# Performance work log

Hardware: AMD Instinct MI355X
Metric: run time of the kernel (lower is better)

Reference implementation:

```python
import jax, jax.numpy as jnp
import numpy as np

N = 20000          # nodes
E = 320000         # edges (avg degree 16)
D_IN, D1, D2, D_OUT = 256, 512, 256, 64
EPS = 1e-5


def _glorot(key, shape):
    lim = (6.0 / (shape[0] + shape[1])) ** 0.5
    return jax.random.uniform(key, shape, jnp.float32, -lim, lim)


def setup_inputs() -> dict:
    key = jax.random.key(0)
    ks = jax.random.split(key, 8)
    x = jax.random.normal(ks[0], (N, D_IN), jnp.float32)
    edge_index = jax.random.randint(ks[1], (2, E), 0, N, dtype=jnp.int64)
    return {
        "x": x,
        "edge_index": edge_index,
        # SAGEConv 1 (SoftmaxAggregation temperature t1 over inp_dim channels)
        "t1": jnp.ones((1, D_IN), jnp.float32),
        "Wl1": _glorot(ks[2], (D_IN, D1)), "bl1": jnp.zeros((D1,), jnp.float32),
        "Wr1": _glorot(ks[3], (D_IN, D1)),
        "g1": jnp.ones((D1,), jnp.float32), "beta1": jnp.zeros((D1,), jnp.float32),
        # SAGEConv 2
        "t2": jnp.ones((1, D1), jnp.float32),
        "Wl2": _glorot(ks[4], (D1, D2)), "bl2": jnp.zeros((D2,), jnp.float32),
        "Wr2": _glorot(ks[5], (D1, D2)),
        "g2": jnp.ones((D2,), jnp.float32), "beta2": jnp.zeros((D2,), jnp.float32),
        # final linear + LayerNorm
        "Wf": _glorot(ks[6], (D2, D_OUT)), "bf": jnp.zeros((D_OUT,), jnp.float32),
        "gx": jnp.ones((D_OUT,), jnp.float32), "betax": jnp.zeros((D_OUT,), jnp.float32),
    }


def _sage_softmax(x, src, dst, t, Wl, bl, Wr, n):
    """SAGEConv with learnable per-channel SoftmaxAggregation."""
    m = x[src]                                              # [E, C] gathered messages
    a = m * t                                               # scaled logits
    amax = jax.ops.segment_max(a, dst, num_segments=n)      # [N, C]
    e = jnp.exp(a - amax[dst])
    denom = jax.ops.segment_sum(e, dst, num_segments=n)     # [N, C]
    w = e / denom[dst]                                      # segment softmax weights
    agg = jax.ops.segment_sum(m * w, dst, num_segments=n)   # weighted neighbor sum
    return agg @ Wl + bl + x @ Wr


def _graph_ln(x, g, b):
    # PyG LayerNorm mode='graph', batch=None: normalize over ALL nodes & channels
    mu = x.mean()
    std = jnp.sqrt(((x - mu) ** 2).mean())
    return (x - mu) / (std + EPS) * g + b


def _ln(x, g, b):
    mu = x.mean(-1, keepdims=True)
    var = ((x - mu) ** 2).mean(-1, keepdims=True)
    return (x - mu) / jnp.sqrt(var + EPS) * g + b


def reference(x, edge_index, t1, Wl1, bl1, Wr1, g1, beta1,
              t2, Wl2, bl2, Wr2, g2, beta2, Wf, bf, gx, betax):
    src, dst = edge_index[0], edge_index[1]
    h = _sage_softmax(x, src, dst, t1, Wl1, bl1, Wr1, N)
    h = jax.nn.relu(_graph_ln(h, g1, beta1))
    h = _sage_softmax(h, src, dst, t2, Wl2, bl2, Wr2, N)
    h = jax.nn.relu(_graph_ln(h, g2, beta2))
    p = h.mean(0, keepdims=True)                            # global_mean_pool, batch=None -> [1, 256]
    out = _ln(p @ Wf + bf, gx, betax)
    return jax.nn.relu(out)
```

## Files before the change

### kernel.cpp

```cpp
#include <hip/hip_runtime.h>
#include <math.h>

#define NODES 20000
#define MPAD  20096
#define EDGES 320000
#define EPSV  1e-5f
#define LOG2E 1.4426950408889634f

#define PREP_CNT   1250
#define PREP_CAST  5000
#define PREP_TR    512
#define PREP_TOTAL (PREP_CNT + PREP_CAST + PREP_TR + 1)

typedef short bf16x8 __attribute__((ext_vector_type(8)));
typedef float f32x4  __attribute__((ext_vector_type(4)));
typedef float f2     __attribute__((ext_vector_type(2)));

__device__ __forceinline__ unsigned short f2bf(float f) {
    unsigned int u = __float_as_uint(f);
    u = (u + 0x7fffu + ((u >> 16) & 1u)) >> 16;
    return (unsigned short)u;
}
__device__ __forceinline__ float bf2f(unsigned short h) {
    return __uint_as_float(((unsigned int)h) << 16);
}

__global__ void k_prep(const int* __restrict__ dst, int* __restrict__ counts,
                       const float* __restrict__ x, unsigned short* __restrict__ xb,
                       const float* __restrict__ Wl1, const float* __restrict__ Wr1,
                       const float* __restrict__ Wl2, const float* __restrict__ Wr2,
                       unsigned short* __restrict__ o1l, unsigned short* __restrict__ o1r,
                       unsigned short* __restrict__ o2l, unsigned short* __restrict__ o2r,
                       float* __restrict__ acc, float* __restrict__ colsum) {
    int b = blockIdx.x;
    int t = threadIdx.x;
    if (b < PREP_CNT) {
        int e = b * 256 + t;
        if (e < EDGES) atomicAdd(&counts[dst[e]], 1);
    } else if (b < PREP_CNT + PREP_CAST) {
        int i = ((b - PREP_CNT) * 256 + t) * 4;
        float4 v = *(const float4*)(x + i);
        xb[i + 0] = f2bf(v.x); xb[i + 1] = f2bf(v.y);
        xb[i + 2] = f2bf(v.z); xb[i + 3] = f2bf(v.w);
    } else if (b < PREP_CNT + PREP_CAST + PREP_TR) {
        __shared__ float tile[32][33];
        int zz = b - PREP_CNT - PREP_CAST;
        int z = zz >> 7;
        int idx = zz & 127;
        const float* W = (z == 0) ? Wl1 : (z == 1) ? Wr1 : (z == 2) ? Wl2 : Wr2;
        unsigned short* Wt = (z == 0) ? o1l : (z == 1) ? o1r : (z == 2) ? o2l : o2r;
        int K = (z < 2) ? 256 : 512, N = (z < 2) ? 512 : 256;
        int nb = N / 32;
        int n0 = (idx % nb) * 32, k0 = (idx / nb) * 32;
        int tx = t & 31, ty = t >> 5;
#pragma unroll
        for (int j = 0; j < 4; j++)
            tile[ty + j * 8][tx] = W[(size_t)(k0 + ty + j * 8) * N + n0 + tx];
        __syncthreads();
#pragma unroll
        for (int j = 0; j < 4; j++)
            Wt[(size_t)(n0 + ty + j * 8) * K + k0 + tx] = f2bf(tile[tx][ty + j * 8]);
    } else {
        if (t < 4) acc[t] = 0.f;
        colsum[t] = 0.f;
    }
}

#define SCAN_B 32

__global__ void k_scan1(const int* __restrict__ counts, int* __restrict__ bsum) {
    __shared__ int sm[256];
    int t = threadIdx.x, b = blockIdx.x;
    int i0 = (b * 256 + t) * 3;
    int s = 0;
#pragma unroll
    for (int j = 0; j < 3; j++) { int i = i0 + j; if (i < NODES) s += counts[i]; }
    sm[t] = s;
    __syncthreads();
    int v = s;
#pragma unroll
    for (int o = 1; o < 256; o <<= 1) {
        int add = (t >= o) ? sm[t - o] : 0;
        __syncthreads();
        v += add;
        sm[t] = v;
        __syncthreads();
    }
    if (t == 255) bsum[b] = v;
}

__global__ void k_scan2(int* __restrict__ bsum, int* __restrict__ offs) {
    int t = threadIdx.x;
    int v = (t < SCAN_B) ? bsum[t] : 0;
    int x = v;
#pragma unroll
    for (int o = 1; o < 64; o <<= 1) {
        int y = __shfl_up(x, o);
        if (t >= o) x += y;
    }
    if (t < SCAN_B) bsum[t] = x - v;
    if (t == SCAN_B - 1) offs[NODES] = x;
}

__global__ void k_scan3(const int* __restrict__ counts, const int* __restrict__ bsum,
                        int* __restrict__ offs) {
    __shared__ int sm[256];
    int t = threadIdx.x, b = blockIdx.x;
    int i0 = (b * 256 + t) * 3;
    int c[3]; int s = 0;
#pragma unroll
    for (int j = 0; j < 3; j++) {
        int i = i0 + j;
        c[j] = (i < NODES) ? counts[i] : 0;
        s += c[j];
    }
    sm[t] = s;
    __syncthreads();
    int v = s;
#pragma unroll
    for (int o = 1; o < 256; o <<= 1) {
        int add = (t >= o) ? sm[t - o] : 0;
        __syncthreads();
        v += add;
        sm[t] = v;
        __syncthreads();
    }
    int run = bsum[b] + (v - s);
#pragma unroll
    for (int j = 0; j < 3; j++) {
        int i = i0 + j;
        if (i < NODES) { offs[i] = run; run += c[j]; }
    }
}

__global__ void k_scatter(const int* __restrict__ src, const int* __restrict__ dst,
                          const int* __restrict__ offs, int* __restrict__ cursor,
                          int* __restrict__ csr_src) {
    int e = blockIdx.x * blockDim.x + threadIdx.x;
    if (e < EDGES) {
        int d = dst[e];
        int pos = atomicAdd(&cursor[d], 1);
        csr_src[offs[d] + pos] = src[e];
    }
}

template <int C, int S, int UNR>
__global__ void k_agg(const unsigned short* __restrict__ xb, const float* __restrict__ tt,
                      const int* __restrict__ offs, const int* __restrict__ csr,
                      unsigned short* __restrict__ out) {
    constexpr int CS  = C / S;
    constexpr int VPL = CS / 64;
    constexpr int W   = VPL / 2;
    typedef unsigned int uv __attribute__((ext_vector_type(W)));
    typedef unsigned short usv __attribute__((ext_vector_type(VPL)));
    int waveg = (int)((blockIdx.x * (unsigned)blockDim.x + threadIdx.x) >> 6);
    int lane = threadIdx.x & 63;
    int node = waveg / S;
    int slice = waveg % S;
    if (node >= NODES) return;
    int beg = __builtin_amdgcn_readfirstlane(offs[node]);
    int end = __builtin_amdgcn_readfirstlane(offs[node + 1]);
    int cb = slice * CS + lane * VPL;
    const unsigned short* __restrict__ xcb = xb + cb;
    f2 tl[W], l[W], s[W];
#pragma unroll
    for (int i = 0; i < W; i++) {
        tl[i][0] = tt[cb + 2 * i] * LOG2E;
        tl[i][1] = tt[cb + 2 * i + 1] * LOG2E;
        l[i][0] = 0.f; l[i][1] = 0.f;
        s[i][0] = 0.f; s[i][1] = 0.f;
    }
    int k = beg;
    for (; k + UNR <= end; k += UNR) {
        uv v[UNR];
#pragma unroll
        for (int u = 0; u < UNR; u++) {
            int sn = csr[k + u];
            v[u] = *(const uv*)(xcb + (size_t)sn * C);
        }
#pragma unroll
        for (int u = 0; u < UNR; u++)
#pragma unroll
            for (int i = 0; i < W; i++) {
                unsigned wd = v[u][i];
                f2 xv;
                xv[0] = __uint_as_float(wd << 16);
                xv[1] = __uint_as_float(wd & 0xffff0000u);
                f2 a = xv * tl[i];
                f2 p;
                p[0] = __builtin_amdgcn_exp2f(a[0]);
                p[1] = __builtin_amdgcn_exp2f(a[1]);
                l[i] += p;
                s[i] = __builtin_elementwise_fma(p, xv, s[i]);
            }
    }
    for (; k < end; k++) {
        int sn = csr[k];
        uv vv = *(const uv*)(xcb + (size_t)sn * C);
#pragma unroll
        for (int i = 0; i < W; i++) {
            unsigned wd = vv[i];
            f2 xv;
            xv[0] = __uint_as_float(wd << 16);
            xv[1] = __uint_as_float(wd & 0xffff0000u);
            f2 a = xv * tl[i];
            f2 p;
            p[0] = __builtin_amdgcn_exp2f(a[0]);
            p[1] = __builtin_amdgcn_exp2f(a[1]);
            l[i] += p;
            s[i] = __builtin_elementwise_fma(p, xv, s[i]);
        }
    }
    bool has = end > beg;
    usv o;
#pragma unroll
    for (int i = 0; i < W; i++) {
        o[2 * i]     = f2bf(has ? s[i][0] / l[i][0] : 0.f);
        o[2 * i + 1] = f2bf(has ? s[i][1] / l[i][1] : 0.f);
    }
    *(usv*)(out + (size_t)node * C + cb) = o;
}

template <int K, int NT, int NTILES, int TN>
__global__ __launch_bounds__(256) void k_gemm_mfma(
    const unsigned short* __restrict__ A1, const unsigned short* __restrict__ B1t,
    const unsigned short* __restrict__ A2, const unsigned short* __restrict__ B2t,
    const float* __restrict__ bias, unsigned short* __restrict__ Co, int M,
    float* __restrict__ stat) {
    constexpr int NF  = TN / 32;
    constexpr int BIT = TN / 64;
    constexpr int HS  = K / 64;
    constexpr int NS  = 2 * HS;
    __shared__ short As[2 * 128 * 32];
    __shared__ short Bs[2 * TN * 32];
    __shared__ float rs[8], rq[8];

    int bx = blockIdx.x;
    int xid = bx & 7, q = bx >> 3;
    int n = q % NTILES, mh = q / NTILES;
    int m = mh * 8 + xid;
    if (m * 128 >= MPAD) return;
    int m0 = m * 128, n0 = n * TN;

    int t = threadIdx.x;
    int wv = t >> 6, lane = t & 63;
    int wm = wv & 1, wn = wv >> 1;
    int lm = lane & 15, quad = lane >> 4;
    int sr = t >> 2;
    int sc8 = (t & 3) * 8;

    f32x4 acc[4][NF] = {};
    bf16x8 rA[2][2];
    bf16x8 rB[2][BIT];

    auto loadslab = [&](int s) {
        const unsigned short* __restrict__ A  = (s < HS) ? A1 : A2;
        const unsigned short* __restrict__ Bt = (s < HS) ? B1t : B2t;
        int kk = (s & (HS - 1)) * 64;
#pragma unroll
        for (int c = 0; c < 2; c++) {
#pragma unroll
            for (int it = 0; it < 2; it++)
                rA[c][it] = *(const bf16x8*)(A + (size_t)(m0 + it * 64 + sr) * K + kk + c * 32 + sc8);
#pragma unroll
            for (int it = 0; it < BIT; it++)
                rB[c][it] = *(const bf16x8*)(Bt + (size_t)(n0 + it * 64 + sr) * K + kk + c * 32 + sc8);
        }
    };

    loadslab(0);
    for (int s = 0; s < NS; s++) {
        if (s) __syncthreads();
#pragma unroll
        for (int c = 0; c < 2; c++) {
#pragma unroll
            for (int it = 0; it < 2; it++)
                *(bf16x8*)&As[c * 4096 + it * 2048 + t * 8] = rA[c][it];
#pragma unroll
            for (int it = 0; it < BIT; it++)
                *(bf16x8*)&Bs[c * (TN * 32) + it * 2048 + t * 8] = rB[c][it];
        }
        __syncthreads();
        if (s + 1 < NS) loadslab(s + 1);
#pragma unroll
        for (int c = 0; c < 2; c++) {
            bf16x8 af[4], bfr[NF];
#pragma unroll
            for (int i = 0; i < 4; i++)
                af[i] = *(const bf16x8*)&As[c * 4096 + (wm * 64 + i * 16 + lm) * 32 + quad * 8];
#pragma unroll
            for (int j = 0; j < NF; j++)
                bfr[j] = *(const bf16x8*)&Bs[c * (TN * 32) + (wn * (TN / 2) + j * 16 + lm) * 32 + quad * 8];
#pragma unroll
            for (int mi = 0; mi < 4; mi++)
#pragma unroll
                for (int nj = 0; nj < NF; nj++)
                    acc[mi][nj] = __builtin_amdgcn_mfma_f32_16x16x32_bf16(
                        af[mi], bfr[nj], acc[mi][nj], 0, 0, 0);
        }
    }

    float sum = 0.f, ss = 0.f;
#pragma unroll
    for (int mi = 0; mi < 4; mi++) {
        int rb = m0 + wm * 64 + mi * 16 + quad * 4;
#pragma unroll
        for (int nj = 0; nj < NF; nj++) {
            int col = n0 + wn * (TN / 2) + nj * 16 + lm;
            float bb = bias[col];
#pragma unroll
            for (int rg = 0; rg < 4; rg++) {
                int row = rb + rg;
                if (row < M) {
                    float y = acc[mi][nj][rg] + bb;
                    Co[(size_t)row * NT + col] = f2bf(y);
                    sum += y; ss += y * y;
                }
            }
        }
    }
#pragma unroll
    for (int o = 32; o > 0; o >>= 1) {
        sum += __shfl_xor(sum, o);
        ss  += __shfl_xor(ss, o);
    }
    if (lane == 0) { rs[wv] = sum; rq[wv] = ss; }
    __syncthreads();
    if (t == 0) {
        float a0 = 0.f, a1 = 0.f;
#pragma unroll
        for (int i = 0; i < 4; i++) { a0 += rs[i] + rs[i + 4]; a1 += rq[i] + rq[i + 4]; }
        atomicAdd(&stat[0], a0); atomicAdd(&stat[1], a1);
    }
}

template <int C>
__global__ void k_ln_relu_b(unsigned short* __restrict__ h, int n,
                            const float* __restrict__ st,
                            const float* __restrict__ g, const float* __restrict__ b) {
    typedef unsigned short us8 __attribute__((ext_vector_type(8)));
    float mu = st[0] / (float)n;
    float var = st[1] / (float)n - mu * mu;
    var = var < 0.f ? 0.f : var;
    float inv = 1.0f / (sqrtf(var) + EPSV);
    int i8 = (blockIdx.x * blockDim.x + threadIdx.x) * 8;
    if (i8 >= n) return;
    int c = i8 & (C - 1);
    us8 v = *(const us8*)(h + i8);
    us8 o;
#pragma unroll
    for (int j = 0; j < 8; j++) {
        float y = (bf2f(v[j]) - mu) * inv * g[c + j] + b[c + j];
        o[j] = f2bf(fmaxf(y, 0.f));
    }
    *(us8*)(h + i8) = o;
}

__global__ void k_ln_colsum(const unsigned short* __restrict__ h, int n,
                            const float* __restrict__ st,
                            const float* __restrict__ g, const float* __restrict__ b,
                            float* __restrict__ colsum) {
    float mu = st[0] / (float)n;
    float var = st[1] / (float)n - mu * mu;
    var = var < 0.f ? 0.f : var;
    float inv = 1.0f / (sqrtf(var) + EPSV);
    int t = threadIdx.x;
    float gv = g[t], bv = b[t];
    float local = 0.f;
    int stride = gridDim.x * blockDim.x;
    for (int i = blockIdx.x * blockDim.x + t; i < n; i += stride) {
        float y = (bf2f(h[i]) - mu) * inv * gv + bv;
        local += fmaxf(y, 0.f);
    }
    atomicAdd(&colsum[t], local);
}

__global__ void k_final(const float* __restrict__ colsum, const float* __restrict__ Wf,
                        const float* __restrict__ bf, const float* __restrict__ gx,
                        const float* __restrict__ bx, float* __restrict__ out) {
    __shared__ float p[256];
    __shared__ float red[4][64];
    int t = threadIdx.x;
    p[t] = colsum[t] * (1.0f / (float)NODES);
    __syncthreads();
    int kg = t >> 6, o = t & 63;
    float a = 0.f;
#pragma unroll
    for (int j = 0; j < 64; j++) {
        int c = kg + j * 4;
        a = fmaf(p[c], Wf[c * 64 + o], a);
    }
    red[kg][o] = a;
    __syncthreads();
    if (t < 64) {
        float acc = bf[t] + red[0][t] + red[1][t] + red[2][t] + red[3][t];
        float sum = acc;
        for (int w = 32; w > 0; w >>= 1) sum += __shfl_xor(sum, w);
        float mu = sum * (1.0f / 64.0f);
        float d = acc - mu;
        float vs = d * d;
        for (int w = 32; w > 0; w >>= 1) vs += __shfl_xor(vs, w);
        float var = vs * (1.0f / 64.0f);
        float y = d * rsqrtf(var + EPSV) * gx[t] + bx[t];
        out[t] = fmaxf(y, 0.f);
    }
}

extern "C" void kernel_launch(void* const* d_in, const int* in_sizes, int n_in,
                              void* d_out, int out_size, void* d_ws, size_t ws_size,
                              hipStream_t stream) {
    const float* x   = (const float*)d_in[0];
    const int*   ei  = (const int*)d_in[1];
    const float* t1  = (const float*)d_in[2];
    const float* Wl1 = (const float*)d_in[3];
    const float* bl1 = (const float*)d_in[4];
    const float* Wr1 = (const float*)d_in[5];
    const float* g1  = (const float*)d_in[6];
    const float* be1 = (const float*)d_in[7];
    const float* t2  = (const float*)d_in[8];
    const float* Wl2 = (const float*)d_in[9];
    const float* bl2 = (const float*)d_in[10];
    const float* Wr2 = (const float*)d_in[11];
    const float* g2  = (const float*)d_in[12];
    const float* be2 = (const float*)d_in[13];
    const float* Wf  = (const float*)d_in[14];
    const float* bf  = (const float*)d_in[15];
    const float* gx  = (const float*)d_in[16];
    const float* bx  = (const float*)d_in[17];
    float* out = (float*)d_out;

    char* ws = (char*)d_ws;
    size_t off = 0;
    auto alloc = [&](size_t bytes) { size_t o = off; off = (off + bytes + 511) & ~511ull; return o; };
    size_t o_counts = alloc((size_t)NODES * 4);
    size_t o_cursor = alloc((size_t)NODES * 4);
    size_t zero_bytes = off;
    size_t o_acc    = alloc(4 * 4);
    size_t o_colsum = alloc(256 * 4);
    size_t o_bsum = alloc((size_t)SCAN_B * 4);
    size_t o_offs = alloc((size_t)(NODES + 1) * 4);
    size_t o_csrc = alloc((size_t)EDGES * 4);
    size_t o_w1l  = alloc((size_t)512 * 256 * 2);
    size_t o_w1r  = alloc((size_t)512 * 256 * 2);
    size_t o_w2l  = alloc((size_t)256 * 512 * 2);
    size_t o_w2r  = alloc((size_t)256 * 512 * 2);
    size_t o_bufX = alloc((size_t)MPAD * 256 * 2);
    size_t o_agg  = alloc((size_t)MPAD * 512 * 2);
    size_t o_h1   = alloc((size_t)(MPAD + 512) * 512 * 2);

    int*   counts = (int*)(ws + o_counts);
    int*   cursor = (int*)(ws + o_cursor);
    float* acc    = (float*)(ws + o_acc);
    float* colsum = (float*)(ws + o_colsum);
    int*   bsum   = (int*)(ws + o_bsum);
    int*   offs   = (int*)(ws + o_offs);
    int*   csrc   = (int*)(ws + o_csrc);
    unsigned short* w1lt = (unsigned short*)(ws + o_w1l);
    unsigned short* w1rt = (unsigned short*)(ws + o_w1r);
    unsigned short* w2lt = (unsigned short*)(ws + o_w2l);
    unsigned short* w2rt = (unsigned short*)(ws + o_w2r);
    unsigned short* xb   = (unsigned short*)(ws + o_bufX);
    unsigned short* h2p  = (unsigned short*)(ws + o_bufX);
    unsigned short* aggb = (unsigned short*)(ws + o_agg);
    unsigned short* h1   = (unsigned short*)(ws + o_h1);

    const int* src = ei;
    const int* dst = ei + EDGES;

    hipMemsetAsync(ws, 0, zero_bytes, stream);

    k_prep<<<PREP_TOTAL, 256, 0, stream>>>(dst, counts, x, xb,
                                           Wl1, Wr1, Wl2, Wr2,
                                           w1lt, w1rt, w2lt, w2rt,
                                           acc, colsum);
    k_scan1<<<SCAN_B, 256, 0, stream>>>(counts, bsum);
    k_scan2<<<1, 64, 0, stream>>>(bsum, offs);
    k_scan3<<<SCAN_B, 256, 0, stream>>>(counts, bsum, offs);
    k_scatter<<<(EDGES + 255) / 256, 256, 0, stream>>>(src, dst, offs, cursor, csrc);

    k_agg<256, 2, 8><<<(NODES * 2 + 3) / 4, 256, 0, stream>>>(xb, t1, offs, csrc, aggb);
    k_gemm_mfma<256, 512, 4, 128><<<8 * 4 * 20, 256, 0, stream>>>(
        aggb, w1lt, xb, w1rt, bl1, h1, NODES, acc);
    k_ln_relu_b<512><<<NODES * 512 / 8 / 256, 256, 0, stream>>>(h1, NODES * 512, acc, g1, be1);

    k_agg<512, 2, 4><<<(NODES * 2 + 3) / 4, 256, 0, stream>>>(h1, t2, offs, csrc, aggb);
    k_gemm_mfma<512, 256, 2, 128><<<8 * 2 * 20, 256, 0, stream>>>(
        aggb, w2lt, h1, w2rt, bl2, h2p, NODES, acc + 2);

    k_ln_colsum<<<1024, 256, 0, stream>>>(h2p, NODES * 256, acc + 2, g2, be2, colsum);
    k_final<<<1, 256, 0, stream>>>(colsum, Wf, bf, gx, bx, out);
}
```

Before: 315.4 us.

## Fuse CSR scan/scatter and final LN/linear into grid-barrier kernels

New measurement: 353.5 us. 12.1% more time.

```diff
diff --git a/kernel.cpp b/kernel.cpp
--- a/kernel.cpp
+++ b/kernel.cpp
@@ -66,15 +66,32 @@
     }
 }
 
-#define SCAN_B 32
-
-__global__ void k_scan1(const int* __restrict__ counts, int* __restrict__ bsum) {
+#define CSR_B 32
+
+__device__ __forceinline__ void grid_bar(int* ctr, int nblk) {
+    __threadfence();
+    __syncthreads();
+    if (threadIdx.x == 0) {
+        __hip_atomic_fetch_add(ctr, 1, __ATOMIC_RELEASE, __HIP_MEMORY_SCOPE_AGENT);
+        while (__hip_atomic_load(ctr, __ATOMIC_ACQUIRE, __HIP_MEMORY_SCOPE_AGENT) < nblk) {}
+    }
+    __syncthreads();
+}
+
+__global__ __launch_bounds__(256) void k_csr(
+    const int* __restrict__ counts, int* __restrict__ bsum, int* __restrict__ offs,
+    const int* __restrict__ src, const int* __restrict__ dst,
+    int* __restrict__ cursor, int* __restrict__ csr_src, int* __restrict__ bar) {
     __shared__ int sm[256];
     int t = threadIdx.x, b = blockIdx.x;
     int i0 = (b * 256 + t) * 3;
-    int s = 0;
-#pragma unroll
-    for (int j = 0; j < 3; j++) { int i = i0 + j; if (i < NODES) s += counts[i]; }
+    int c[3]; int s = 0;
+#pragma unroll
+    for (int j = 0; j < 3; j++) {
+        int i = i0 + j;
+        c[j] = (i < NODES) ? counts[i] : 0;
+        s += c[j];
+    }
     sm[t] = s;
     __syncthreads();
     int v = s;
@@ -87,57 +104,18 @@
         __syncthreads();
     }
     if (t == 255) bsum[b] = v;
-}
-
-__global__ void k_scan2(int* __restrict__ bsum, int* __restrict__ offs) {
-    int t = threadIdx.x;
-    int v = (t < SCAN_B) ? bsum[t] : 0;
-    int x = v;
-#pragma unroll
-    for (int o = 1; o < 64; o <<= 1) {
-        int y = __shfl_up(x, o);
-        if (t >= o) x += y;
-    }
-    if (t < SCAN_B) bsum[t] = x - v;
-    if (t == SCAN_B - 1) offs[NODES] = x;
-}
-
-__global__ void k_scan3(const int* __restrict__ counts, const int* __restrict__ bsum,
-                        int* __restrict__ offs) {
-    __shared__ int sm[256];
-    int t = threadIdx.x, b = blockIdx.x;
-    int i0 = (b * 256 + t) * 3;
-    int c[3]; int s = 0;
-#pragma unroll
-    for (int j = 0; j < 3; j++) {
-        int i = i0 + j;
-        c[j] = (i < NODES) ? counts[i] : 0;
-        s += c[j];
-    }
-    sm[t] = s;
-    __syncthreads();
-    int v = s;
-#pragma unroll
-    for (int o = 1; o < 256; o <<= 1) {
-        int add = (t >= o) ? sm[t - o] : 0;
-        __syncthreads();
-        v += add;
-        sm[t] = v;
-        __syncthreads();
-    }
-    int run = bsum[b] + (v - s);
+    grid_bar(&bar[0], CSR_B);
+    int base = 0;
+    for (int i = 0; i < b; i++) base += bsum[i];
+    if (b == CSR_B - 1 && t == 255) offs[NODES] = base + v;
+    int run = base + (v - s);
 #pragma unroll
     for (int j = 0; j < 3; j++) {
         int i = i0 + j;
         if (i < NODES) { offs[i] = run; run += c[j]; }
     }
-}
-
-__global__ void k_scatter(const int* __restrict__ src, const int* __restrict__ dst,
-                          const int* __restrict__ offs, int* __restrict__ cursor,
-                          int* __restrict__ csr_src) {
-    int e = blockIdx.x * blockDim.x + threadIdx.x;
-    if (e < EDGES) {
+    grid_bar(&bar[1], CSR_B);
+    for (int e = b * 256 + t; e < EDGES; e += CSR_B * 256) {
         int d = dst[e];
         int pos = atomicAdd(&cursor[d], 1);
         csr_src[offs[d] + pos] = src[e];
@@ -233,7 +211,7 @@
     constexpr int NS  = 2 * HS;
     __shared__ short As[2 * 128 * 32];
     __shared__ short Bs[2 * TN * 32];
-    __shared__ float rs[8], rq[8];
+    __shared__ float rs[4], rq[4];
 
     int bx = blockIdx.x;
     int xid = bx & 7, q = bx >> 3;
@@ -329,7 +307,7 @@
     if (t == 0) {
         float a0 = 0.f, a1 = 0.f;
 #pragma unroll
-        for (int i = 0; i < 4; i++) { a0 += rs[i] + rs[i + 4]; a1 += rq[i] + rq[i + 4]; }
+        for (int i = 0; i < 4; i++) { a0 += rs[i]; a1 += rq[i]; }
         atomicAdd(&stat[0], a0); atomicAdd(&stat[1], a1);
     }
 }
@@ -356,10 +334,14 @@
     *(us8*)(h + i8) = o;
 }
 
-__global__ void k_ln_colsum(const unsigned short* __restrict__ h, int n,
-                            const float* __restrict__ st,
-                            const float* __restrict__ g, const float* __restrict__ b,
-                            float* __restrict__ colsum) {
+__global__ __launch_bounds__(256) void k_lncol_final(
+    const unsigned short* __restrict__ h, int n, const float* __restrict__ st,
+    const float* __restrict__ g, const float* __restrict__ b,
+    float* __restrict__ colsum, const float* __restrict__ Wf,
+    const float* __restrict__ bf, const float* __restrict__ gx,
+    const float* __restrict__ bx, float* __restrict__ out, int* __restrict__ bar) {
+    __shared__ float p[256];
+    __shared__ float red[4][64];
     float mu = st[0] / (float)n;
     float var = st[1] / (float)n - mu * mu;
     var = var < 0.f ? 0.f : var;
@@ -373,14 +355,14 @@
         local += fmaxf(y, 0.f);
     }
     atomicAdd(&colsum[t], local);
-}
-
-__global__ void k_final(const float* __restrict__ colsum, const float* __restrict__ Wf,
-                        const float* __restrict__ bf, const float* __restrict__ gx,
-                        const float* __restrict__ bx, float* __restrict__ out) {
-    __shared__ float p[256];
-    __shared__ float red[4][64];
-    int t = threadIdx.x;
+    __threadfence();
+    __syncthreads();
+    if (t == 0)
+        __hip_atomic_fetch_add(&bar[2], 1, __ATOMIC_RELEASE, __HIP_MEMORY_SCOPE_AGENT);
+    if (blockIdx.x != 0) return;
+    if (t == 0)
+        while (__hip_atomic_load(&bar[2], __ATOMIC_ACQUIRE, __HIP_MEMORY_SCOPE_AGENT) < (int)gridDim.x) {}
+    __syncthreads();
     p[t] = colsum[t] * (1.0f / (float)NODES);
     __syncthreads();
     int kg = t >> 6, o = t & 63;
@@ -396,12 +378,12 @@
         float acc = bf[t] + red[0][t] + red[1][t] + red[2][t] + red[3][t];
         float sum = acc;
         for (int w = 32; w > 0; w >>= 1) sum += __shfl_xor(sum, w);
-        float mu = sum * (1.0f / 64.0f);
-        float d = acc - mu;
+        float muh = sum * (1.0f / 64.0f);
+        float d = acc - muh;
         float vs = d * d;
         for (int w = 32; w > 0; w >>= 1) vs += __shfl_xor(vs, w);
-        float var = vs * (1.0f / 64.0f);
-        float y = d * rsqrtf(var + EPSV) * gx[t] + bx[t];
+        float varh = vs * (1.0f / 64.0f);
+        float y = d * rsqrtf(varh + EPSV) * gx[t] + bx[t];
         out[t] = fmaxf(y, 0.f);
     }
 }
@@ -434,10 +416,11 @@
     auto alloc = [&](size_t bytes) { size_t o = off; off = (off + bytes + 511) & ~511ull; return o; };
     size_t o_counts = alloc((size_t)NODES * 4);
     size_t o_cursor = alloc((size_t)NODES * 4);
+    size_t o_bar    = alloc(16 * 4);
     size_t zero_bytes = off;
     size_t o_acc    = alloc(4 * 4);
     size_t o_colsum = alloc(256 * 4);
-    size_t o_bsum = alloc((size_t)SCAN_B * 4);
+    size_t o_bsum = alloc((size_t)CSR_B * 4);
     size_t o_offs = alloc((size_t)(NODES + 1) * 4);
     size_t o_csrc = alloc((size_t)EDGES * 4);
     size_t o_w1l  = alloc((size_t)512 * 256 * 2);
@@ -450,6 +433,7 @@
 
     int*   counts = (int*)(ws + o_counts);
     int*   cursor = (int*)(ws + o_cursor);
+    int*   bar    = (int*)(ws + o_bar);
     float* acc    = (float*)(ws + o_acc);
     float* colsum = (float*)(ws + o_colsum);
     int*   bsum   = (int*)(ws + o_bsum);
@@ -473,10 +457,7 @@
                                            Wl1, Wr1, Wl2, Wr2,
                                            w1lt, w1rt, w2lt, w2rt,
                                            acc, colsum);
-    k_scan1<<<SCAN_B, 256, 0, stream>>>(counts, bsum);
-    k_scan2<<<1, 64, 0, stream>>>(bsum, offs);
-    k_scan3<<<SCAN_B, 256, 0, stream>>>(counts, bsum, offs);
-    k_scatter<<<(EDGES + 255) / 256, 256, 0, stream>>>(src, dst, offs, cursor, csrc);
+    k_csr<<<CSR_B, 256, 0, stream>>>(counts, bsum, offs, src, dst, cursor, csrc, bar);
 
     k_agg<256, 2, 8><<<(NODES * 2 + 3) / 4, 256, 0, stream>>>(xb, t1, offs, csrc, aggb);
     k_gemm_mfma<256, 512, 4, 128><<<8 * 4 * 20, 256, 0, stream>>>(
@@ -487,6 +468,6 @@
     k_gemm_mfma<512, 256, 2, 128><<<8 * 2 * 20, 256, 0, stream>>>(
         aggb, w2lt, h1, w2rt, bl2, h2p, NODES, acc + 2);
 
-    k_ln_colsum<<<1024, 256, 0, stream>>>(h2p, NODES * 256, acc + 2, g2, be2, colsum);
-    k_final<<<1, 256, 0, stream>>>(colsum, Wf, bf, gx, bx, out);
-}
+    k_lncol_final<<<256, 256, 0, stream>>>(h2p, NODES * 256, acc + 2, g2, be2,
+                                           colsum, Wf, bf, gx, bx, out, bar);
+}
```
